# Kernel tuning notes

Hardware: AMD Instinct MI355X
Metric: run time of the kernel (lower is better)

The kernel has to match this reference:

```python
import jax, jax.numpy as jnp
import numpy as np

B, S, H, NCOL, NH = 32, 512, 768, 32, 12
HD = H // NH  # head dim 64
LN_EPS = 1e-12


def setup_inputs() -> dict:
    key = jax.random.key(0)
    ks = jax.random.split(key, 20)
    s = 0.02
    inp = {
        'hidden_states': jax.random.normal(ks[0], (B, S, H), jnp.float32),
        'column_embeddings': jax.random.normal(ks[1], (B, NCOL, H), jnp.float32),
        'column_categories': jax.random.randint(ks[2], (B, NCOL), 0, 2, jnp.int32),
        'value_mask': jax.random.randint(ks[3], (B, S), 0, NCOL + 1, jnp.int32),
        'Wd': jax.random.normal(ks[4], (H, H), jnp.float32) * s,
        'bd': jnp.zeros((H,), jnp.float32),
        'Wc': jax.random.normal(ks[5], (H, H), jnp.float32) * s,
        'bc': jnp.zeros((H,), jnp.float32),
        'Wq': jax.random.normal(ks[6], (H, H), jnp.float32) * s,
        'bq': jnp.zeros((H,), jnp.float32),
        'Wk': jax.random.normal(ks[7], (H, H), jnp.float32) * s,
        'bk': jnp.zeros((H,), jnp.float32),
        'Wv': jax.random.normal(ks[8], (H, H), jnp.float32) * s,
        'bv': jnp.zeros((H,), jnp.float32),
        'Wo': jax.random.normal(ks[9], (H, H), jnp.float32) * s,
        'bo': jnp.zeros((H,), jnp.float32),
        'ln_g': jnp.ones((H,), jnp.float32),
        'ln_b': jnp.zeros((H,), jnp.float32),
    }
    return inp


def _layernorm(x, g, b):
    mu = jnp.mean(x, axis=-1, keepdims=True)
    var = jnp.mean(jnp.square(x - mu), axis=-1, keepdims=True)
    return (x - mu) * jax.lax.rsqrt(var + LN_EPS) * g + b


def reference(hidden_states, column_embeddings, column_categories, value_mask,
              Wd, bd, Wc, bc, Wq, bq, Wk, bk, Wv, bv, Wo, bo, ln_g, ln_b):
    # dense branch
    h_ = hidden_states @ Wd.T + bd  # [B,S,H]
    # column gather: zero out category==0 columns, prepend zero row for index 0
    table = column_embeddings * (column_categories == 1)[..., None].astype(column_embeddings.dtype)
    table = jnp.concatenate([jnp.zeros_like(table[:, :1]), table], axis=1)  # [B,NCOL+1,H]
    h_col = jnp.take_along_axis(table, value_mask[..., None].astype(jnp.int32), axis=1)  # [B,S,H]
    h = jax.nn.gelu(h_ + (h_col @ Wc.T + bc), approximate=False)
    # Roberta self-attention
    def heads(x):
        return x.reshape(B, S, NH, HD).transpose(0, 2, 1, 3)  # [B,NH,S,HD]
    q = heads(h @ Wq.T + bq)
    k = heads(h @ Wk.T + bk)
    v = heads(h @ Wv.T + bv)
    scores = jnp.einsum('bhsd,bhtd->bhst', q, k) / jnp.sqrt(jnp.float32(HD))
    probs = jax.nn.softmax(scores, axis=-1)
    ctx = jnp.einsum('bhst,bhtd->bhsd', probs, v).transpose(0, 2, 1, 3).reshape(B, S, H)
    # self-output: dense + residual + layernorm
    out = _layernorm(ctx @ Wo.T + bo + h, ln_g, ln_b)
    return out
```

## Files before the change

kernel.cpp:

```cpp
#include <hip/hip_runtime.h>
#include <hip/hip_bf16.h>
#include <math.h>
#include <stdint.h>

#define B_    32
#define S_    512
#define H_    768
#define NH_   12
#define HD_   64
#define NCOL_ 32
#define M_    (B_*S_)

typedef __bf16 bf16;
typedef __bf16 bf16x8 __attribute__((ext_vector_type(8)));
typedef __bf16 bf16x4 __attribute__((ext_vector_type(4)));
typedef float  f32x4  __attribute__((ext_vector_type(4)));

__device__ __forceinline__ void async_load16(const void* g, void* l) {
    __builtin_amdgcn_global_load_lds(
        (__attribute__((address_space(1))) unsigned int*)g,
        (__attribute__((address_space(3))) unsigned int*)l, 16, 0, 0);
}

__device__ __forceinline__ bf16x8 cvt8(const float* p) {
    const float4* fp = (const float4*)p;
    float4 x = fp[0], y = fp[1];
    bf16x8 r;
    r[0] = (bf16)x.x; r[1] = (bf16)x.y; r[2] = (bf16)x.z; r[3] = (bf16)x.w;
    r[4] = (bf16)y.x; r[5] = (bf16)y.y; r[6] = (bf16)y.z; r[7] = (bf16)y.w;
    return r;
}

__global__ __launch_bounds__(256) void cvt_x_kernel(
    const float* __restrict__ hidden, const float* __restrict__ ce,
    const int* __restrict__ cc, const int* __restrict__ vm,
    bf16* __restrict__ hbf, bf16* __restrict__ hcol)
{
    int id = blockIdx.x * 256 + threadIdx.x;
    if (id < M_ * 96) {
        int row = id / 96, c = id - row * 96;
        *(bf16x8*)&hbf[(long)row * H_ + c * 8] = cvt8(hidden + (long)row * H_ + c * 8);
    } else {
        int cid = id - M_ * 96;
        int row = cid / 96, c = cid - row * 96;
        int b = row >> 9;
        int m = vm[row];
        bf16x8 val;
#pragma unroll
        for (int i = 0; i < 8; i++) val[i] = (bf16)0.0f;
        if (m > 0) {
            int col = m - 1;
            if (cc[b * NCOL_ + col] == 1)
                val = cvt8(ce + ((long)(b * NCOL_ + col)) * H_ + c * 8);
        }
        *(bf16x8*)&hcol[(long)row * H_ + c * 8] = val;
    }
}

__global__ __launch_bounds__(256) void cvt_w_kernel(
    const float* __restrict__ Wd, const float* __restrict__ Wc,
    const float* __restrict__ Wq, const float* __restrict__ Wk,
    const float* __restrict__ Wv, const float* __restrict__ Wo,
    const float* __restrict__ bq, const float* __restrict__ bk,
    const float* __restrict__ bv, bf16* __restrict__ wpack,
    float* __restrict__ bqkv)
{
    int id = blockIdx.x * 256 + threadIdx.x;
    if (id < 442368) {
        const float* src;
        int r = id;
        if      (r < 73728)  { src = Wd; }
        else if (r < 147456) { src = Wc; r -= 73728; }
        else if (r < 221184) { src = Wq; r -= 147456; }
        else if (r < 294912) { src = Wk; r -= 221184; }
        else if (r < 368640) { src = Wv; r -= 294912; }
        else                 { src = Wo; r -= 368640; }
        *(bf16x8*)&wpack[(long)id * 8] = cvt8(src + (long)r * 8);
    } else if (id < 442656) {
        int j0 = (id - 442368) * 8;
#pragma unroll
        for (int i = 0; i < 8; i++) {
            int j = j0 + i;
            float v = (j < 768) ? bq[j] : (j < 1536) ? bk[j - 768] : bv[j - 1536];
            bqkv[j] = v;
        }
    }
}

template<int MODE>
__global__ __launch_bounds__(256) void gemm_bt(
    const bf16* __restrict__ A0, const bf16* __restrict__ A1,
    const bf16* __restrict__ B0, const bf16* __restrict__ B1,
    const float* __restrict__ bias1, const float* __restrict__ bias2,
    const bf16* __restrict__ resid, bf16* __restrict__ out,
    int K, int KSPLIT)
{
    __shared__ __align__(16) bf16 As[128 * 32];
    __shared__ __align__(16) bf16 Bs[128 * 32];

    const int tid  = threadIdx.x;
    const int lane = tid & 63;
    const int wave = tid >> 6;
    const int wm   = wave & 1;
    const int wn   = wave >> 1;
    const int m0   = blockIdx.x * 128;
    const int n0   = blockIdx.y * 128;

    const int srow = tid >> 2;
    const int scol = (tid & 3) * 8;

    f32x4 acc[4][4];
    const f32x4 zero4 = {0.f, 0.f, 0.f, 0.f};
#pragma unroll
    for (int i = 0; i < 4; i++)
#pragma unroll
        for (int j = 0; j < 4; j++) acc[i][j] = zero4;

    const int a_off = (wm * 64 + (lane & 15)) * 32 + (lane >> 4) * 8;
    const int b_off = (wn * 64 + (lane & 15)) * 32 + (lane >> 4) * 8;

    for (int k0 = 0; k0 < K; k0 += 32) {
        const bf16* ag;
        const bf16* bg;
        if (k0 < KSPLIT) { ag = A0 + k0; bg = B0 + k0; }
        else             { ag = A1 + (k0 - KSPLIT); bg = B1 + (k0 - KSPLIT); }

        __syncthreads();
        async_load16(ag + (long)(m0 + srow) * H_ + scol,       As + tid * 8);
        async_load16(ag + (long)(m0 + 64 + srow) * H_ + scol,  As + 2048 + tid * 8);
        async_load16(bg + (long)(n0 + srow) * H_ + scol,       Bs + tid * 8);
        async_load16(bg + (long)(n0 + 64 + srow) * H_ + scol,  Bs + 2048 + tid * 8);
        __syncthreads();

        bf16x8 af[4], bfr[4];
#pragma unroll
        for (int i = 0; i < 4; i++) af[i]  = *(const bf16x8*)(As + a_off + i * 512);
#pragma unroll
        for (int j = 0; j < 4; j++) bfr[j] = *(const bf16x8*)(Bs + b_off + j * 512);
#pragma unroll
        for (int i = 0; i < 4; i++)
#pragma unroll
            for (int j = 0; j < 4; j++)
                acc[i][j] = __builtin_amdgcn_mfma_f32_16x16x32_bf16(af[i], bfr[j], acc[i][j], 0, 0, 0);
    }

    const int c_r = (lane >> 4) * 4;
    const int c_c = lane & 15;

    int sec = 0;
    if (MODE == 1) sec = (n0 >= 1536) ? 2 : ((n0 >= 768) ? 1 : 0);
    bf16* dst = (MODE == 1) ? out + (long)sec * M_ * H_ : out;

#pragma unroll
    for (int j = 0; j < 4; j++) {
        const int col = n0 + wn * 64 + j * 16 + c_c;
        float bias = bias1[col];
        if (MODE == 0) bias += bias2[col];
#pragma unroll
        for (int i = 0; i < 4; i++) {
#pragma unroll
            for (int r = 0; r < 4; r++) {
                const int row = m0 + wm * 64 + i * 16 + c_r + r;
                float v = acc[i][j][r] + bias;
                if (MODE == 0) {
                    v = 0.5f * v * (1.0f + erff(v * 0.70710678118654752f));
                    dst[(long)row * H_ + col] = (bf16)v;
                } else if (MODE == 1) {
                    int b = row >> 9, s = row & 511;
                    int cs = col - sec * 768;
                    int head = cs >> 6, d = cs & 63;
                    if (sec == 2)
                        dst[(((long)(b * NH_ + head)) * HD_ + d) * S_ + s] = (bf16)v;
                    else
                        dst[(((long)(b * NH_ + head)) * S_ + s) * HD_ + d] = (bf16)v;
                } else {
                    v += (float)resid[(long)row * H_ + col];
                    dst[(long)row * H_ + col] = (bf16)v;
                }
            }
        }
    }
}

#define QP 72

__global__ __launch_bounds__(256) void attn_kernel(
    const bf16* __restrict__ q, const bf16* __restrict__ k,
    const bf16* __restrict__ vt, bf16* __restrict__ ctx)
{
    __shared__ __align__(16) bf16 Qs[64 * QP];
    __shared__ __align__(16) bf16 Ks[64 * QP];
    __shared__ __align__(16) bf16 Vt[64 * QP];
    __shared__ __align__(16) bf16 Ps[4][16 * QP];

    const int tid  = threadIdx.x;
    const int lane = tid & 63;
    const int w    = tid >> 6;
    const int quad = lane >> 4;
    const int ln16 = lane & 15;

    const int bid = blockIdx.x;
    const int qt  = bid / 384;
    const int g   = bid - qt * 384;
    const int b   = g / 12;
    const int h   = g - b * 12;
    const long base = ((long)(b * NH_ + h)) * S_ * HD_;

    const int r0 = tid >> 2;
    const int e0 = (tid & 3) * 16;

    {
        const bf16* qg = q + base + (long)qt * 64 * HD_;
        *(uint4*)&Qs[r0 * QP + e0]     = *(const uint4*)&qg[r0 * HD_ + e0];
        *(uint4*)&Qs[r0 * QP + e0 + 8] = *(const uint4*)&qg[r0 * HD_ + e0 + 8];
    }
    const bf16* kg = k  + base;
    const bf16* vg = vt + base;
    uint4 kr0 = *(const uint4*)&kg[r0 * HD_ + e0];
    uint4 kr1 = *(const uint4*)&kg[r0 * HD_ + e0 + 8];
    uint4 vr0 = *(const uint4*)&vg[(long)r0 * S_ + e0];
    uint4 vr1 = *(const uint4*)&vg[(long)r0 * S_ + e0 + 8];
    __syncthreads();

    const bf16x8 bq0 = *(const bf16x8*)&Qs[(w * 16 + ln16) * QP + quad * 8];
    const bf16x8 bq1 = *(const bf16x8*)&Qs[(w * 16 + ln16) * QP + 32 + quad * 8];

    f32x4 O[4];
    const f32x4 zero4 = {0.f, 0.f, 0.f, 0.f};
#pragma unroll
    for (int t = 0; t < 4; t++) O[t] = zero4;
    float mo = -1e30f, l = 0.f;

    for (int kc = 0; kc < 8; kc++) {
        __syncthreads();
        *(uint4*)&Ks[r0 * QP + e0]     = kr0;
        *(uint4*)&Ks[r0 * QP + e0 + 8] = kr1;
        *(uint4*)&Vt[r0 * QP + e0]     = vr0;
        *(uint4*)&Vt[r0 * QP + e0 + 8] = vr1;
        {
            int kcn = (kc < 7) ? kc + 1 : 7;
            kr0 = *(const uint4*)&kg[(long)kcn * 64 * HD_ + r0 * HD_ + e0];
            kr1 = *(const uint4*)&kg[(long)kcn * 64 * HD_ + r0 * HD_ + e0 + 8];
            vr0 = *(const uint4*)&vg[(long)r0 * S_ + kcn * 64 + e0];
            vr1 = *(const uint4*)&vg[(long)r0 * S_ + kcn * 64 + e0 + 8];
        }
        __syncthreads();

        f32x4 sc[4];
#pragma unroll
        for (int i = 0; i < 4; i++) {
            bf16x8 a0 = *(const bf16x8*)&Ks[(i * 16 + ln16) * QP + quad * 8];
            bf16x8 a1 = *(const bf16x8*)&Ks[(i * 16 + ln16) * QP + 32 + quad * 8];
            sc[i] = zero4;
            sc[i] = __builtin_amdgcn_mfma_f32_16x16x32_bf16(a0, bq0, sc[i], 0, 0, 0);
            sc[i] = __builtin_amdgcn_mfma_f32_16x16x32_bf16(a1, bq1, sc[i], 0, 0, 0);
        }

        float cm = -1e30f;
#pragma unroll
        for (int i = 0; i < 4; i++)
#pragma unroll
            for (int r = 0; r < 4; r++) {
                float s = sc[i][r] * 0.125f;
                sc[i][r] = s;
                cm = fmaxf(cm, s);
            }
        cm = fmaxf(cm, __shfl_xor(cm, 16));
        cm = fmaxf(cm, __shfl_xor(cm, 32));
        float mn = fmaxf(mo, cm);
        float alpha = __expf(mo - mn);
        float rs = 0.f;
#pragma unroll
        for (int i = 0; i < 4; i++) {
            bf16x4 pk;
#pragma unroll
            for (int r = 0; r < 4; r++) {
                float p = __expf(sc[i][r] - mn);
                rs += p;
                pk[r] = (bf16)p;
            }
            *(bf16x4*)&Ps[w][ln16 * QP + i * 16 + quad * 4] = pk;
        }
        rs += __shfl_xor(rs, 16);
        rs += __shfl_xor(rs, 32);
        l  = l * alpha + rs;
        mo = mn;
#pragma unroll
        for (int t = 0; t < 4; t++)
#pragma unroll
            for (int r = 0; r < 4; r++) O[t][r] *= alpha;

        bf16x8 bp0 = *(const bf16x8*)&Ps[w][ln16 * QP + quad * 8];
        bf16x8 bp1 = *(const bf16x8*)&Ps[w][ln16 * QP + 32 + quad * 8];
#pragma unroll
        for (int dt = 0; dt < 4; dt++) {
            bf16x8 a0 = *(const bf16x8*)&Vt[(dt * 16 + ln16) * QP + quad * 8];
            bf16x8 a1 = *(const bf16x8*)&Vt[(dt * 16 + ln16) * QP + 32 + quad * 8];
            O[dt] = __builtin_amdgcn_mfma_f32_16x16x32_bf16(a0, bp0, O[dt], 0, 0, 0);
            O[dt] = __builtin_amdgcn_mfma_f32_16x16x32_bf16(a1, bp1, O[dt], 0, 0, 0);
        }
    }

    {
        float inv = 1.0f / l;
#pragma unroll
        for (int dt = 0; dt < 4; dt++) {
            bf16x4 ov;
#pragma unroll
            for (int r = 0; r < 4; r++) ov[r] = (bf16)(O[dt][r] * inv);
            *(bf16x4*)&Qs[(w * 16 + ln16) * QP + dt * 16 + quad * 4] = ov;
        }
    }
    __syncthreads();
    {
        uint4 o0 = *(const uint4*)&Qs[r0 * QP + e0];
        uint4 o1 = *(const uint4*)&Qs[r0 * QP + e0 + 8];
        bf16* cg = ctx + ((long)(b * S_ + qt * 64 + r0)) * H_ + h * HD_;
        *(uint4*)&cg[e0]     = o0;
        *(uint4*)&cg[e0 + 8] = o1;
    }
}

__global__ __launch_bounds__(256) void ln_kernel(
    const bf16* __restrict__ y, const float* __restrict__ g,
    const float* __restrict__ be, float* __restrict__ out)
{
    const int lane = threadIdx.x & 63;
    const int w    = threadIdx.x >> 6;
    const long row = (long)blockIdx.x * 4 + w;
    const bf16* yr = y + row * H_;

    float x[12];
    float sum = 0.f, ss = 0.f;
#pragma unroll
    for (int j = 0; j < 12; j++) {
        x[j] = (float)yr[j * 64 + lane];
        sum += x[j];
        ss  += x[j] * x[j];
    }
#pragma unroll
    for (int m = 1; m < 64; m <<= 1) {
        sum += __shfl_xor(sum, m);
        ss  += __shfl_xor(ss, m);
    }
    const float mu  = sum * (1.0f / 768.0f);
    float var = ss * (1.0f / 768.0f) - mu * mu;
    const float rs = rsqrtf(fmaxf(var, 0.f) + 1e-12f);
#pragma unroll
    for (int j = 0; j < 12; j++) {
        int c = j * 64 + lane;
        out[row * H_ + c] = (x[j] - mu) * rs * g[c] + be[c];
    }
}

extern "C" void kernel_launch(void* const* d_in, const int* in_sizes, int n_in,
                              void* d_out, int out_size, void* d_ws, size_t ws_size,
                              hipStream_t stream)
{
    const float* hidden = (const float*)d_in[0];
    const float* ce     = (const float*)d_in[1];
    const int*   cc     = (const int*)d_in[2];
    const int*   vm     = (const int*)d_in[3];
    const float* Wd     = (const float*)d_in[4];
    const float* bd     = (const float*)d_in[5];
    const float* Wc     = (const float*)d_in[6];
    const float* bc     = (const float*)d_in[7];
    const float* Wq     = (const float*)d_in[8];
    const float* bq     = (const float*)d_in[9];
    const float* Wk     = (const float*)d_in[10];
    const float* bk     = (const float*)d_in[11];
    const float* Wv     = (const float*)d_in[12];
    const float* bv     = (const float*)d_in[13];
    const float* Wo     = (const float*)d_in[14];
    const float* bo     = (const float*)d_in[15];
    const float* lng    = (const float*)d_in[16];
    const float* lnb    = (const float*)d_in[17];

    const long NE = (long)M_ * H_;
    bf16* ws   = (bf16*)d_ws;
    bf16* hbuf = ws;
    bf16* qkv  = ws + NE;
    bf16* hbf  = qkv;
    bf16* hcol = qkv + NE;
    bf16* qb   = qkv;
    bf16* kb   = qkv + NE;
    bf16* vb   = qkv + 2 * NE;
    bf16* wpack = ws + 4 * NE;
    const bf16* Wd_b  = wpack;
    const bf16* Wc_b  = wpack + 589824;
    const bf16* Wq_b  = wpack + 1179648;
    const bf16* Wk_b  = wpack + 1769472;
    const bf16* Wv_b  = wpack + 2359296;
    const bf16* Wo_b  = wpack + 2949120;
    float* bqkv = (float*)(wpack + 3538944);
    bf16* ctx = (bf16*)d_out;

    cvt_x_kernel<<<2 * M_ * 96 / 256, 256, 0, stream>>>(hidden, ce, cc, vm, hbf, hcol);
    cvt_w_kernel<<<1730, 256, 0, stream>>>(Wd, Wc, Wq, Wk, Wv, Wo, bq, bk, bv, wpack, bqkv);

    dim3 g6(M_ / 128, 6);
    dim3 g18(M_ / 128, 18);
    gemm_bt<0><<<g6, 256, 0, stream>>>(hbf, hcol, Wd_b, Wc_b, bd, bc, nullptr, hbuf, 2 * H_, H_);
    gemm_bt<1><<<g18, 256, 0, stream>>>(hbuf, hbuf, Wq_b, Wq_b, bqkv, nullptr, nullptr, qkv, H_, 3 * H_);
    attn_kernel<<<3072, 256, 0, stream>>>(qb, kb, vb, ctx);
    gemm_bt<2><<<g6, 256, 0, stream>>>(ctx, ctx, Wo_b, Wo_b, bo, nullptr, hbuf, hbuf, H_, H_);
    ln_kernel<<<M_ / 4, 256, 0, stream>>>(hbuf, lng, lnb, (float*)d_out);
}
```

Measured before the change: 430.9 us.

## Double-buffer GEMM LDS tiles, vectorize V-transpose stores, merge conversion kernels

The GEMM now keeps two LDS buffers and issues the async global-to-LDS loads for the next K tile before computing the current one. This removes one barrier per iteration and is meant to overlap memory latency with MFMA work. The transposed V output writes four consecutive sequence positions as a single bf16x4 store instead of four scalar stores. The input and weight conversion kernels are merged into one launch. The extra LDS buffer doubles shared memory per block, which may lower occupancy. Correctness relies on the single barrier at the top of the loop also ordering the async load completion.

Result: faster. 397.1 us (-7.8%).

```diff
diff --git a/kernel.cpp b/kernel.cpp
--- a/kernel.cpp
+++ b/kernel.cpp
@@ -31,18 +31,25 @@
     return r;
 }
 
-__global__ __launch_bounds__(256) void cvt_x_kernel(
+__global__ __launch_bounds__(256) void cvt_kernel(
     const float* __restrict__ hidden, const float* __restrict__ ce,
     const int* __restrict__ cc, const int* __restrict__ vm,
-    bf16* __restrict__ hbf, bf16* __restrict__ hcol)
+    const float* __restrict__ Wd, const float* __restrict__ Wc,
+    const float* __restrict__ Wq, const float* __restrict__ Wk,
+    const float* __restrict__ Wv, const float* __restrict__ Wo,
+    const float* __restrict__ bq, const float* __restrict__ bk,
+    const float* __restrict__ bv,
+    bf16* __restrict__ hbf, bf16* __restrict__ hcol,
+    bf16* __restrict__ wpack, float* __restrict__ bqkv)
 {
-    int id = blockIdx.x * 256 + threadIdx.x;
-    if (id < M_ * 96) {
+    int blk = blockIdx.x;
+    if (blk < 6144) {
+        int id = blk * 256 + threadIdx.x;
         int row = id / 96, c = id - row * 96;
         *(bf16x8*)&hbf[(long)row * H_ + c * 8] = cvt8(hidden + (long)row * H_ + c * 8);
-    } else {
-        int cid = id - M_ * 96;
-        int row = cid / 96, c = cid - row * 96;
+    } else if (blk < 12288) {
+        int id = (blk - 6144) * 256 + threadIdx.x;
+        int row = id / 96, c = id - row * 96;
         int b = row >> 9;
         int m = vm[row];
         bf16x8 val;
@@ -54,35 +61,26 @@
                 val = cvt8(ce + ((long)(b * NCOL_ + col)) * H_ + c * 8);
         }
         *(bf16x8*)&hcol[(long)row * H_ + c * 8] = val;
-    }
-}
-
-__global__ __launch_bounds__(256) void cvt_w_kernel(
-    const float* __restrict__ Wd, const float* __restrict__ Wc,
-    const float* __restrict__ Wq, const float* __restrict__ Wk,
-    const float* __restrict__ Wv, const float* __restrict__ Wo,
-    const float* __restrict__ bq, const float* __restrict__ bk,
-    const float* __restrict__ bv, bf16* __restrict__ wpack,
-    float* __restrict__ bqkv)
-{
-    int id = blockIdx.x * 256 + threadIdx.x;
-    if (id < 442368) {
-        const float* src;
-        int r = id;
-        if      (r < 73728)  { src = Wd; }
-        else if (r < 147456) { src = Wc; r -= 73728; }
-        else if (r < 221184) { src = Wq; r -= 147456; }
-        else if (r < 294912) { src = Wk; r -= 221184; }
-        else if (r < 368640) { src = Wv; r -= 294912; }
-        else                 { src = Wo; r -= 368640; }
-        *(bf16x8*)&wpack[(long)id * 8] = cvt8(src + (long)r * 8);
-    } else if (id < 442656) {
-        int j0 = (id - 442368) * 8;
-#pragma unroll
-        for (int i = 0; i < 8; i++) {
-            int j = j0 + i;
-            float v = (j < 768) ? bq[j] : (j < 1536) ? bk[j - 768] : bv[j - 1536];
-            bqkv[j] = v;
+    } else {
+        int id = (blk - 12288) * 256 + threadIdx.x;
+        if (id < 442368) {
+            const float* src;
+            int r = id;
+            if      (r < 73728)  { src = Wd; }
+            else if (r < 147456) { src = Wc; r -= 73728; }
+            else if (r < 221184) { src = Wq; r -= 147456; }
+            else if (r < 294912) { src = Wk; r -= 221184; }
+            else if (r < 368640) { src = Wv; r -= 294912; }
+            else                 { src = Wo; r -= 368640; }
+            *(bf16x8*)&wpack[(long)id * 8] = cvt8(src + (long)r * 8);
+        } else if (id < 442656) {
+            int j0 = (id - 442368) * 8;
+#pragma unroll
+            for (int i = 0; i < 8; i++) {
+                int j = j0 + i;
+                float v = (j < 768) ? bq[j] : (j < 1536) ? bk[j - 768] : bv[j - 1536];
+                bqkv[j] = v;
+            }
         }
     }
 }
@@ -95,8 +93,8 @@
     const bf16* __restrict__ resid, bf16* __restrict__ out,
     int K, int KSPLIT)
 {
-    __shared__ __align__(16) bf16 As[128 * 32];
-    __shared__ __align__(16) bf16 Bs[128 * 32];
+    __shared__ __align__(16) bf16 As[2][128 * 32];
+    __shared__ __align__(16) bf16 Bs[2][128 * 32];
 
     const int tid  = threadIdx.x;
     const int lane = tid & 63;
@@ -119,24 +117,26 @@
     const int a_off = (wm * 64 + (lane & 15)) * 32 + (lane >> 4) * 8;
     const int b_off = (wn * 64 + (lane & 15)) * 32 + (lane >> 4) * 8;
 
-    for (int k0 = 0; k0 < K; k0 += 32) {
-        const bf16* ag;
-        const bf16* bg;
-        if (k0 < KSPLIT) { ag = A0 + k0; bg = B0 + k0; }
-        else             { ag = A1 + (k0 - KSPLIT); bg = B1 + (k0 - KSPLIT); }
-
+    auto stage = [&](int kk, int buf) {
+        const bf16* ag = (kk < KSPLIT) ? A0 + kk : A1 + (kk - KSPLIT);
+        const bf16* bg = (kk < KSPLIT) ? B0 + kk : B1 + (kk - KSPLIT);
+        async_load16(ag + (long)(m0 + srow) * H_ + scol,      &As[buf][tid * 8]);
+        async_load16(ag + (long)(m0 + 64 + srow) * H_ + scol, &As[buf][2048 + tid * 8]);
+        async_load16(bg + (long)(n0 + srow) * H_ + scol,      &Bs[buf][tid * 8]);
+        async_load16(bg + (long)(n0 + 64 + srow) * H_ + scol, &Bs[buf][2048 + tid * 8]);
+    };
+
+    stage(0, 0);
+    int cur = 0;
+    for (int k0 = 0; k0 < K; k0 += 32, cur ^= 1) {
         __syncthreads();
-        async_load16(ag + (long)(m0 + srow) * H_ + scol,       As + tid * 8);
-        async_load16(ag + (long)(m0 + 64 + srow) * H_ + scol,  As + 2048 + tid * 8);
-        async_load16(bg + (long)(n0 + srow) * H_ + scol,       Bs + tid * 8);
-        async_load16(bg + (long)(n0 + 64 + srow) * H_ + scol,  Bs + 2048 + tid * 8);
-        __syncthreads();
+        if (k0 + 32 < K) stage(k0 + 32, cur ^ 1);
 
         bf16x8 af[4], bfr[4];
 #pragma unroll
-        for (int i = 0; i < 4; i++) af[i]  = *(const bf16x8*)(As + a_off + i * 512);
-#pragma unroll
-        for (int j = 0; j < 4; j++) bfr[j] = *(const bf16x8*)(Bs + b_off + j * 512);
+        for (int i = 0; i < 4; i++) af[i]  = *(const bf16x8*)(&As[cur][a_off + i * 512]);
+#pragma unroll
+        for (int j = 0; j < 4; j++) bfr[j] = *(const bf16x8*)(&Bs[cur][b_off + j * 512]);
 #pragma unroll
         for (int i = 0; i < 4; i++)
 #pragma unroll
@@ -158,24 +158,32 @@
         if (MODE == 0) bias += bias2[col];
 #pragma unroll
         for (int i = 0; i < 4; i++) {
-#pragma unroll
-            for (int r = 0; r < 4; r++) {
-                const int row = m0 + wm * 64 + i * 16 + c_r + r;
-                float v = acc[i][j][r] + bias;
-                if (MODE == 0) {
-                    v = 0.5f * v * (1.0f + erff(v * 0.70710678118654752f));
-                    dst[(long)row * H_ + col] = (bf16)v;
-                } else if (MODE == 1) {
-                    int b = row >> 9, s = row & 511;
-                    int cs = col - sec * 768;
-                    int head = cs >> 6, d = cs & 63;
-                    if (sec == 2)
-                        dst[(((long)(b * NH_ + head)) * HD_ + d) * S_ + s] = (bf16)v;
-                    else
+            if (MODE == 1 && sec == 2) {
+                const int row0 = m0 + wm * 64 + i * 16 + c_r;
+                int b = row0 >> 9, s = row0 & 511;
+                int cs = col - 1536;
+                int head = cs >> 6, d = cs & 63;
+                bf16x4 pk;
+#pragma unroll
+                for (int r = 0; r < 4; r++) pk[r] = (bf16)(acc[i][j][r] + bias);
+                *(bf16x4*)&dst[(((long)(b * NH_ + head)) * HD_ + d) * S_ + s] = pk;
+            } else {
+#pragma unroll
+                for (int r = 0; r < 4; r++) {
+                    const int row = m0 + wm * 64 + i * 16 + c_r + r;
+                    float v = acc[i][j][r] + bias;
+                    if (MODE == 0) {
+                        v = 0.5f * v * (1.0f + erff(v * 0.70710678118654752f));
+                        dst[(long)row * H_ + col] = (bf16)v;
+                    } else if (MODE == 1) {
+                        int b = row >> 9, s = row & 511;
+                        int cs = col - sec * 768;
+                        int head = cs >> 6, d = cs & 63;
                         dst[(((long)(b * NH_ + head)) * S_ + s) * HD_ + d] = (bf16)v;
-                } else {
-                    v += (float)resid[(long)row * H_ + col];
-                    dst[(long)row * H_ + col] = (bf16)v;
+                    } else {
+                        v += (float)resid[(long)row * H_ + col];
+                        dst[(long)row * H_ + col] = (bf16)v;
+                    }
                 }
             }
         }
@@ -395,8 +403,8 @@
     float* bqkv = (float*)(wpack + 3538944);
     bf16* ctx = (bf16*)d_out;
 
-    cvt_x_kernel<<<2 * M_ * 96 / 256, 256, 0, stream>>>(hidden, ce, cc, vm, hbf, hcol);
-    cvt_w_kernel<<<1730, 256, 0, stream>>>(Wd, Wc, Wq, Wk, Wv, Wo, bq, bk, bv, wpack, bqkv);
+    cvt_kernel<<<14018, 256, 0, stream>>>(hidden, ce, cc, vm, Wd, Wc, Wq, Wk, Wv, Wo,
+                                          bq, bk, bv, hbf, hcol, wpack, bqkv);
 
     dim3 g6(M_ / 128, 6);
     dim3 g18(M_ / 128, 18);
```
